# Kernel optimization log

Measured on AMD Instinct MI355X. Metric: run time of the kernel, lower is better.

Reference implementation:

```python
import jax, jax.numpy as jnp
import numpy as np
import math

H = 8      # n_heads
D = 64     # d_model (per-head dim in this module)
QDIM = 512


def setup_inputs() -> dict:
    key = jax.random.key(0)
    ks = jax.random.split(key, 11)
    B, L = 4, 1024
    s = 1.0 / math.sqrt(QDIM)
    inp = {
        "q": jax.random.normal(ks[0], (B, L, QDIM), jnp.float32),
        "k": jax.random.normal(ks[1], (B, L, QDIM), jnp.float32),
        "v": jax.random.normal(ks[2], (B, L, QDIM), jnp.float32),
        # Linear weights (torch layout: [out, in]); biases init to zeros in original
        "wq": jax.random.normal(ks[3], (H * D, QDIM), jnp.float32) * s,
        "bq": jnp.zeros((H * D,), jnp.float32),
        "wk": jax.random.normal(ks[4], (H * D, QDIM), jnp.float32) * s,
        "bk": jnp.zeros((H * D,), jnp.float32),
        "wv": jax.random.normal(ks[5], (H * D, QDIM), jnp.float32) * s,
        "bv": jnp.zeros((H * D,), jnp.float32),
        "wp": jax.random.normal(ks[6], (D, H * D), jnp.float32) * (1.0 / math.sqrt(H * D)),
        "bp": jnp.zeros((D,), jnp.float32),
    }
    return inp


def reference(q, k, v, wq, bq, wk, bk, wv, bv, wp, bp):
    b = q.shape[0]
    # projections, split into heads: [b, L, H, D] -> [b, H, L, D]
    q_s = (q @ wq.T + bq).reshape(b, -1, H, D).transpose(0, 2, 1, 3)
    k_s = (k @ wk.T + bk).reshape(b, -1, H, D).transpose(0, 2, 1, 3)
    v_s = (v @ wv.T + bv).reshape(b, -1, H, D).transpose(0, 2, 1, 3)
    # NOTE: original scales by sqrt(batch_size), not sqrt(d_k)
    scores = jnp.einsum("bhqd,bhkd->bhqk", q_s, k_s) / math.sqrt(b)
    attn = jax.nn.softmax(scores, axis=-1)
    # context = attn^T @ v  (quirk: output seq length = k_len)
    context = jnp.einsum("bhqk,bhqd->bhkd", attn, v_s)
    context = context.transpose(0, 2, 1, 3).reshape(b, -1, H * D)
    output = context @ wp.T + bp  # dropout is identity at eval
    return (output, attn)
```

## Files before the change

### kernel.cpp

```cpp
#include <hip/hip_runtime.h>

#define QD 512
#define NW (512*512)

typedef __attribute__((ext_vector_type(8))) short bf16x8;
typedef __attribute__((ext_vector_type(4))) short bf16x4;
typedef __attribute__((ext_vector_type(4))) float f32x4;

#define MFMA16(a,b,c) __builtin_amdgcn_mfma_f32_16x16x32_bf16((a),(b),(c),0,0,0)

static __device__ __forceinline__ short f2bf(float f) {
  unsigned u = __float_as_uint(f);
  u += 0x7fffu + ((u >> 16) & 1u);
  return (short)(u >> 16);
}
static __device__ __forceinline__ float bf2f(short s) {
  return __uint_as_float(((unsigned)(unsigned short)s) << 16);
}
static __device__ __forceinline__ unsigned pk2(float a, float b) {
  return (unsigned)(unsigned short)f2bf(a) | (((unsigned)(unsigned short)f2bf(b)) << 16);
}

#define GL2LDS16(g, l)                                                        \
  __builtin_amdgcn_global_load_lds(                                           \
      (const __attribute__((address_space(1))) unsigned int*)(g),             \
      (__attribute__((address_space(3))) unsigned int*)(l), 16, 0, 0)

__global__ __launch_bounds__(256) void k_wconv(
    const float* __restrict__ wq, const float* __restrict__ wk,
    const float* __restrict__ wv, const float* __restrict__ wp,
    short* __restrict__ W, short* __restrict__ WPH) {
  int i = blockIdx.x * 256 + threadIdx.x;
  if (i < NW) {
    float f = wq[i]; short h = f2bf(f);
    W[i] = h; W[NW + i] = f2bf(f - bf2f(h));
  } else if (i < 2 * NW) {
    int j = i - NW;
    float f = wk[j]; short h = f2bf(f);
    W[2 * NW + j] = h; W[3 * NW + j] = f2bf(f - bf2f(h));
  } else if (i < 3 * NW) {
    int j = i - 2 * NW;
    W[4 * NW + j] = f2bf(wv[j]);
  } else {
    int j = i - 3 * NW;
    if (j < 64 * QD) WPH[j] = f2bf(wp[j]);
  }
}

__global__ __launch_bounds__(256) void k_xconv(
    const float* __restrict__ q, const float* __restrict__ k, const float* __restrict__ v,
    short* __restrict__ XqH, short* __restrict__ XqL,
    short* __restrict__ XkH, short* __restrict__ XkL, short* __restrict__ XvH) {
  int i = blockIdx.x * 256 + threadIdx.x;
  int t = i >> 18;
  int j = i & 0x3FFFF;
  const float* src = t == 0 ? q : (t == 1 ? k : v);
  f32x4 x0 = *(const f32x4*)(src + (size_t)j * 8);
  f32x4 x1 = *(const f32x4*)(src + (size_t)j * 8 + 4);
  bf16x8 H, L;
#pragma unroll
  for (int jj = 0; jj < 4; ++jj) {
    short h0 = f2bf(x0[jj]); H[jj] = h0; L[jj] = f2bf(x0[jj] - bf2f(h0));
    short h1 = f2bf(x1[jj]); H[jj + 4] = h1; L[jj + 4] = f2bf(x1[jj] - bf2f(h1));
  }
  if (t == 0)      { *(bf16x8*)(XqH + (size_t)j * 8) = H; *(bf16x8*)(XqL + (size_t)j * 8) = L; }
  else if (t == 1) { *(bf16x8*)(XkH + (size_t)j * 8) = H; *(bf16x8*)(XkL + (size_t)j * 8) = L; }
  else             { *(bf16x8*)(XvH + (size_t)j * 8) = H; }
}

__global__ __launch_bounds__(256) void k_proj(
    const short* __restrict__ XH, const short* __restrict__ XL,
    const short* __restrict__ WH, const short* __restrict__ WL,
    const float* __restrict__ bias,
    short* __restrict__ outH, short* __restrict__ outL,
    short* __restrict__ Vt, int mode, float scale) {
  __shared__ __align__(16) short Ah[64 * 32], Al[64 * 32], Bh[64 * 32], Bl[64 * 32];
  const int tid = threadIdx.x;
  const int lane = tid & 63;
  const int col = lane & 15, g = lane >> 4;
  const int w = tid >> 6, wr = w >> 1, wc = w & 1;
  const int h = blockIdx.x;
  const int m0 = blockIdx.y * 64;
  const int srow = tid >> 2;
  const int scol = ((tid & 3) ^ (srow & 3)) * 8;
  const size_t xrow = (size_t)(m0 + srow) * QD + scol;
  const size_t wrow = (size_t)(h * 64 + srow) * QD + scol;

  f32x4 zero = {0.f, 0.f, 0.f, 0.f};
  f32x4 acc[2][2] = {{zero, zero}, {zero, zero}};

  for (int kc = 0; kc < 16; ++kc) {
    const int kb = kc * 32;
    GL2LDS16(XH + xrow + kb, &Ah[tid * 8]);
    GL2LDS16(WH + wrow + kb, &Bh[tid * 8]);
    if (mode == 0) {
      GL2LDS16(XL + xrow + kb, &Al[tid * 8]);
      GL2LDS16(WL + wrow + kb, &Bl[tid * 8]);
    }
    __syncthreads();

    bf16x8 a_h[2], a_l[2], b_h[2], b_l[2];
#pragma unroll
    for (int mt = 0; mt < 2; ++mt) {
      int rowa = wr * 32 + mt * 16 + col;
      int off = rowa * 32 + ((g ^ (rowa & 3)) * 8);
      a_h[mt] = *(const bf16x8*)&Ah[off];
      if (mode == 0) a_l[mt] = *(const bf16x8*)&Al[off];
    }
#pragma unroll
    for (int nt = 0; nt < 2; ++nt) {
      int rowb = wc * 32 + nt * 16 + col;
      int off = rowb * 32 + ((g ^ (rowb & 3)) * 8);
      b_h[nt] = *(const bf16x8*)&Bh[off];
      if (mode == 0) b_l[nt] = *(const bf16x8*)&Bl[off];
    }
#pragma unroll
    for (int mt = 0; mt < 2; ++mt)
#pragma unroll
      for (int nt = 0; nt < 2; ++nt) {
        acc[mt][nt] = MFMA16(a_h[mt], b_h[nt], acc[mt][nt]);
        if (mode == 0) {
          acc[mt][nt] = MFMA16(a_l[mt], b_h[nt], acc[mt][nt]);
          acc[mt][nt] = MFMA16(a_h[mt], b_l[nt], acc[mt][nt]);
        }
      }
    __syncthreads();
  }

#pragma unroll
  for (int nt = 0; nt < 2; ++nt) {
    int d = wc * 32 + nt * 16 + col;
    float bias_v = bias[h * 64 + d];
#pragma unroll
    for (int mt = 0; mt < 2; ++mt)
#pragma unroll
      for (int r = 0; r < 4; ++r) {
        int m = m0 + wr * 32 + mt * 16 + g * 4 + r;
        int b = m >> 10, l = m & 1023;
        float val = (acc[mt][nt][r] + bias_v) * scale;
        if (mode == 0) {
          size_t idx = (((size_t)b * 8 + h) * 1024 + l) * 64 + d;
          short hh = f2bf(val);
          outH[idx] = hh;
          outL[idx] = f2bf(val - bf2f(hh));
        } else {
          Vt[(((size_t)b * 8 + h) * 64 + d) * 1024 + l] = f2bf(val);
        }
      }
  }
}

__global__ __launch_bounds__(256) void k_sums(
    const short* __restrict__ QsH, const short* __restrict__ KsH,
    float* __restrict__ invp) {
  __shared__ __align__(16) short KL[32 * 64];
  const int tid = threadIdx.x;
  const int lane = tid & 63, w = tid >> 6;
  const int col = lane & 15, g = lane >> 4;
  int wgid = blockIdx.x + gridDim.x * blockIdx.y;
  int nid = (wgid & 7) * 64 + (wgid >> 3);
  const int qblk = nid & 15, bh = nid >> 4;
  const int q0 = qblk * 64 + w * 16;
  const size_t base = (size_t)bh * 65536;

  const short* qp = QsH + base + (size_t)(q0 + col) * 64 + g * 8;
  bf16x8 qB0 = *(const bf16x8*)qp;
  bf16x8 qB1 = *(const bf16x8*)(qp + 32);

  const int srow = tid >> 3, sslot = tid & 7;
  const short* ksrc = KsH + base + (size_t)srow * 64 + ((sslot ^ (srow & 7)) * 8);

  f32x4 zero = {0.f, 0.f, 0.f, 0.f};
  float sum = 0.f;
  for (int kb = 0; kb < 32; ++kb) {
    GL2LDS16(ksrc + kb * 2048, &KL[tid * 8]);
    __syncthreads();
#pragma unroll
    for (int sub = 0; sub < 2; ++sub) {
      const short* lb = &KL[(sub * 16 + col) * 64];
      bf16x8 ka0 = *(const bf16x8*)(lb + ((g ^ (col & 7)) * 8));
      bf16x8 ka1 = *(const bf16x8*)(lb + (((4 + g) ^ (col & 7)) * 8));
      f32x4 S = zero;
      S = MFMA16(ka0, qB0, S);
      S = MFMA16(ka1, qB1, S);
      sum += __expf(S[0]) + __expf(S[1]) + __expf(S[2]) + __expf(S[3]);
    }
    __syncthreads();
  }
  sum += __shfl_xor(sum, 16);
  sum += __shfl_xor(sum, 32);
  if (lane < 16) invp[bh * 1024 + q0 + col] = 1.f / sum;
}

__global__ __launch_bounds__(256) void k_pv(
    const short* __restrict__ QsH, const short* __restrict__ QsL,
    const short* __restrict__ KsH, const short* __restrict__ KsL,
    const short* __restrict__ Vt, const float* __restrict__ invp,
    float* __restrict__ attn, short* __restrict__ ctx) {
  __shared__ __align__(16) short QH[32 * 64], QL[32 * 64];
  const int tid = threadIdx.x;
  const int lane = tid & 63, w = tid >> 6;
  const int col = lane & 15, g = lane >> 4;
  int wgid = blockIdx.x + gridDim.x * blockIdx.y;
  int nid = (wgid & 7) * 64 + (wgid >> 3);
  const int kblk = nid & 15, bh = nid >> 4;
  const int k0 = kblk * 64 + w * 16;
  const size_t base = (size_t)bh * 65536;

  const short* kp = KsH + base + (size_t)(k0 + col) * 64 + g * 8;
  bf16x8 khB0 = *(const bf16x8*)kp;
  bf16x8 khB1 = *(const bf16x8*)(kp + 32);
  const short* kpl = KsL + base + (size_t)(k0 + col) * 64 + g * 8;
  bf16x8 klB0 = *(const bf16x8*)kpl;
  bf16x8 klB1 = *(const bf16x8*)(kpl + 32);

  const short* vb = Vt + base;
  float* ab = attn + (size_t)bh * 1024 * 1024;
  const float* invB = invp + bh * 1024;

  const int srow = tid >> 3, sslot = tid & 7;
  const size_t qsrc = base + (size_t)srow * 64 + ((sslot ^ (srow & 7)) * 8);

  f32x4 zero = {0.f, 0.f, 0.f, 0.f};
  f32x4 O[4] = {zero, zero, zero, zero};

  for (int cc = 0; cc < 32; ++cc) {
    GL2LDS16(QsH + qsrc + cc * 2048, &QH[tid * 8]);
    GL2LDS16(QsL + qsrc + cc * 2048, &QL[tid * 8]);
    __syncthreads();

    float p[2][4];
#pragma unroll
    for (int t = 0; t < 2; ++t) {
      const short* lh = &QH[(t * 16 + col) * 64];
      const short* ll = &QL[(t * 16 + col) * 64];
      int o0 = (g ^ (col & 7)) * 8, o1 = ((4 + g) ^ (col & 7)) * 8;
      bf16x8 qh0 = *(const bf16x8*)(lh + o0);
      bf16x8 qh1 = *(const bf16x8*)(lh + o1);
      bf16x8 ql0 = *(const bf16x8*)(ll + o0);
      bf16x8 ql1 = *(const bf16x8*)(ll + o1);
      f32x4 S = zero;
      S = MFMA16(qh0, khB0, S);
      S = MFMA16(qh1, khB1, S);
      S = MFMA16(ql0, khB0, S);
      S = MFMA16(ql1, khB1, S);
      S = MFMA16(qh0, klB0, S);
      S = MFMA16(qh1, klB1, S);
      f32x4 iv = *(const f32x4*)(invB + cc * 32 + t * 16 + 4 * g);
      float* ap = ab + (size_t)(cc * 32 + t * 16 + 4 * g) * 1024 + k0 + col;
#pragma unroll
      for (int r = 0; r < 4; ++r) {
        p[t][r] = __expf(S[r]) * iv[r];
        ap[(size_t)r * 1024] = p[t][r];
      }
    }
    union { bf16x8 v; unsigned u[4]; } pa;
    pa.u[0] = pk2(p[0][0], p[0][1]); pa.u[1] = pk2(p[0][2], p[0][3]);
    pa.u[2] = pk2(p[1][0], p[1][1]); pa.u[3] = pk2(p[1][2], p[1][3]);
#pragma unroll
    for (int dt = 0; dt < 4; ++dt) {
      const short* vr = vb + (size_t)(dt * 16 + col) * 1024 + cc * 32 + 4 * g;
      union { bf16x8 v; bf16x4 h[2]; } vf;
      vf.h[0] = *(const bf16x4*)vr;
      vf.h[1] = *(const bf16x4*)(vr + 16);
      O[dt] = MFMA16(pa.v, vf.v, O[dt]);
    }
    __syncthreads();
  }

  int b = bh >> 3, h = bh & 7;
#pragma unroll
  for (int dt = 0; dt < 4; ++dt)
#pragma unroll
    for (int r = 0; r < 4; ++r) {
      int kk = k0 + 4 * g + r;
      ctx[((size_t)(b * 1024 + kk)) * 512 + h * 64 + dt * 16 + col] = f2bf(O[dt][r]);
    }
}

__global__ __launch_bounds__(256) void k_out(
    const short* __restrict__ ctx, const short* __restrict__ WPH,
    const float* __restrict__ bp, float* __restrict__ out) {
  const int lane = threadIdx.x & 63, w = threadIdx.x >> 6;
  const int col = lane & 15, g = lane >> 4;
  const int m0 = blockIdx.x * 64 + w * 16;

  f32x4 zero = {0.f, 0.f, 0.f, 0.f};
  f32x4 acc[4] = {zero, zero, zero, zero};

  for (int kc = 0; kc < 16; ++kc) {
    bf16x8 a = *(const bf16x8*)(ctx + (size_t)(m0 + col) * 512 + kc * 32 + g * 8);
#pragma unroll
    for (int nt = 0; nt < 4; ++nt) {
      bf16x8 bfr = *(const bf16x8*)(WPH + (size_t)(nt * 16 + col) * 512 + kc * 32 + g * 8);
      acc[nt] = MFMA16(a, bfr, acc[nt]);
    }
  }
#pragma unroll
  for (int nt = 0; nt < 4; ++nt) {
    float bias = bp[nt * 16 + col];
#pragma unroll
    for (int r = 0; r < 4; ++r)
      out[(size_t)(m0 + g * 4 + r) * 64 + nt * 16 + col] = acc[nt][r] + bias;
  }
}

extern "C" void kernel_launch(void* const* d_in, const int* in_sizes, int n_in,
                              void* d_out, int out_size, void* d_ws, size_t ws_size,
                              hipStream_t stream) {
  const float* q  = (const float*)d_in[0];
  const float* k  = (const float*)d_in[1];
  const float* v  = (const float*)d_in[2];
  const float* wq = (const float*)d_in[3];
  const float* bq = (const float*)d_in[4];
  const float* wk = (const float*)d_in[5];
  const float* bk = (const float*)d_in[6];
  const float* wv = (const float*)d_in[7];
  const float* bv = (const float*)d_in[8];
  const float* wp = (const float*)d_in[9];
  const float* bp = (const float*)d_in[10];

  float* out  = (float*)d_out;
  float* attn = out + 262144;

  short* S = (short*)d_ws;
  const size_t E = 2097152;
  short* XqH = S;
  short* XqL = S + E;
  short* XkH = S + 2 * E;
  short* XkL = S + 3 * E;
  short* XvH = S + 4 * E;
  short* QsH = S + 5 * E;
  short* QsL = S + 6 * E;
  short* KsH = S;
  short* KsL = S + E;
  short* Vt  = S + 2 * E;
  short* ctx = S + 3 * E;
  short* W   = S + 7 * E;
  short* WPH = W + 5 * (size_t)NW;
  float* invp = (float*)(WPH + 64 * QD);

  k_wconv<<<dim3(3200), dim3(256), 0, stream>>>(wq, wk, wv, wp, W, WPH);
  k_xconv<<<dim3(3072), dim3(256), 0, stream>>>(q, k, v, XqH, XqL, XkH, XkL, XvH);
  k_proj <<<dim3(8, 64), dim3(256), 0, stream>>>(XqH, XqL, W, W + NW, bq,
                                                 QsH, QsL, nullptr, 0, 0.5f);
  k_proj <<<dim3(8, 64), dim3(256), 0, stream>>>(XkH, XkL, W + 2 * NW, W + 3 * NW, bk,
                                                 KsH, KsL, nullptr, 0, 1.0f);
  k_proj <<<dim3(8, 64), dim3(256), 0, stream>>>(XvH, XvH, W + 4 * NW, W + 4 * NW, bv,
                                                 nullptr, nullptr, Vt, 1, 1.0f);
  k_sums <<<dim3(16, 32), dim3(256), 0, stream>>>(QsH, KsH, invp);
  k_pv   <<<dim3(16, 32), dim3(256), 0, stream>>>(QsH, QsL, KsH, KsL, Vt, invp,
                                                  attn, ctx);
  k_out  <<<dim3(64), dim3(256), 0, stream>>>(ctx, WPH, bp, out);
}
```

Before: 305.8 us.

## Split softmax sums and PV over key/query chunks, reduce partial contexts

The row-sum kernel is split four ways along the key dimension, with partial sums combined through atomics and inverted in a new small kernel. The PV kernel is split along the query dimension into up to four fp32 partial context buffers, chosen by available workspace, and a new reduction kernel adds them and writes hi/lo bf16 context. The output projection now uses a three-term split-bf16 product for higher precision. This raises grid sizes from 512 blocks so more CUs are busy, at the cost of extra launches, a memset, atomics and extra fp32 traffic.

Result: slower. 319.5 us (+4.5%).

```diff
diff --git a/kernel.cpp b/kernel.cpp
--- a/kernel.cpp
+++ b/kernel.cpp
@@ -29,7 +29,7 @@
 __global__ __launch_bounds__(256) void k_wconv(
     const float* __restrict__ wq, const float* __restrict__ wk,
     const float* __restrict__ wv, const float* __restrict__ wp,
-    short* __restrict__ W, short* __restrict__ WPH) {
+    short* __restrict__ W, short* __restrict__ WPH, short* __restrict__ WPL) {
   int i = blockIdx.x * 256 + threadIdx.x;
   if (i < NW) {
     float f = wq[i]; short h = f2bf(f);
@@ -43,7 +43,10 @@
     W[4 * NW + j] = f2bf(wv[j]);
   } else {
     int j = i - 3 * NW;
-    if (j < 64 * QD) WPH[j] = f2bf(wp[j]);
+    if (j < 64 * QD) {
+      float f = wp[j]; short h = f2bf(f);
+      WPH[j] = h; WPL[j] = f2bf(f - bf2f(h));
+    }
   }
 }
 
@@ -152,7 +155,7 @@
 
 __global__ __launch_bounds__(256) void k_sums(
     const short* __restrict__ QsH, const short* __restrict__ KsH,
-    float* __restrict__ invp) {
+    float* __restrict__ sums) {
   __shared__ __align__(16) short KL[32 * 64];
   const int tid = threadIdx.x;
   const int lane = tid & 63, w = tid >> 6;
@@ -160,6 +163,7 @@
   int wgid = blockIdx.x + gridDim.x * blockIdx.y;
   int nid = (wgid & 7) * 64 + (wgid >> 3);
   const int qblk = nid & 15, bh = nid >> 4;
+  const int kq = blockIdx.z;
   const int q0 = qblk * 64 + w * 16;
   const size_t base = (size_t)bh * 65536;
 
@@ -168,11 +172,12 @@
   bf16x8 qB1 = *(const bf16x8*)(qp + 32);
 
   const int srow = tid >> 3, sslot = tid & 7;
-  const short* ksrc = KsH + base + (size_t)srow * 64 + ((sslot ^ (srow & 7)) * 8);
+  const short* ksrc = KsH + base + (size_t)(kq * 256 + srow) * 64 +
+                      ((sslot ^ (srow & 7)) * 8);
 
   f32x4 zero = {0.f, 0.f, 0.f, 0.f};
   float sum = 0.f;
-  for (int kb = 0; kb < 32; ++kb) {
+  for (int kb = 0; kb < 8; ++kb) {
     GL2LDS16(ksrc + kb * 2048, &KL[tid * 8]);
     __syncthreads();
 #pragma unroll
@@ -189,14 +194,21 @@
   }
   sum += __shfl_xor(sum, 16);
   sum += __shfl_xor(sum, 32);
-  if (lane < 16) invp[bh * 1024 + q0 + col] = 1.f / sum;
+  if (lane < 16) atomicAdd(&sums[bh * 1024 + q0 + col], sum);
+}
+
+__global__ __launch_bounds__(256) void k_inv(float* __restrict__ s) {
+  int i = blockIdx.x * 256 + threadIdx.x;
+  s[i] = 1.f / s[i];
 }
 
 __global__ __launch_bounds__(256) void k_pv(
     const short* __restrict__ QsH, const short* __restrict__ QsL,
     const short* __restrict__ KsH, const short* __restrict__ KsL,
     const short* __restrict__ Vt, const float* __restrict__ invp,
-    float* __restrict__ attn, short* __restrict__ ctx) {
+    float* __restrict__ attn,
+    float* __restrict__ c0, float* __restrict__ c1,
+    float* __restrict__ c2, float* __restrict__ c3, int cpb) {
   __shared__ __align__(16) short QH[32 * 64], QL[32 * 64];
   const int tid = threadIdx.x;
   const int lane = tid & 63, w = tid >> 6;
@@ -204,6 +216,8 @@
   int wgid = blockIdx.x + gridDim.x * blockIdx.y;
   int nid = (wgid & 7) * 64 + (wgid >> 3);
   const int kblk = nid & 15, bh = nid >> 4;
+  const int qc = blockIdx.z;
+  float* ctxP = qc == 0 ? c0 : (qc == 1 ? c1 : (qc == 2 ? c2 : c3));
   const int k0 = kblk * 64 + w * 16;
   const size_t base = (size_t)bh * 65536;
 
@@ -224,7 +238,8 @@
   f32x4 zero = {0.f, 0.f, 0.f, 0.f};
   f32x4 O[4] = {zero, zero, zero, zero};
 
-  for (int cc = 0; cc < 32; ++cc) {
+  for (int ci = 0; ci < cpb; ++ci) {
+    const int cc = qc * cpb + ci;
     GL2LDS16(QsH + qsrc + cc * 2048, &QH[tid * 8]);
     GL2LDS16(QsL + qsrc + cc * 2048, &QL[tid * 8]);
     __syncthreads();
@@ -274,12 +289,33 @@
 #pragma unroll
     for (int r = 0; r < 4; ++r) {
       int kk = k0 + 4 * g + r;
-      ctx[((size_t)(b * 1024 + kk)) * 512 + h * 64 + dt * 16 + col] = f2bf(O[dt][r]);
-    }
+      ctxP[((size_t)(b * 1024 + kk)) * 512 + h * 64 + dt * 16 + col] = O[dt][r];
+    }
+}
+
+__global__ __launch_bounds__(256) void k_red(
+    const float* __restrict__ c0, const float* __restrict__ c1,
+    const float* __restrict__ c2, const float* __restrict__ c3, int nc,
+    short* __restrict__ ctxH, short* __restrict__ ctxL) {
+  size_t i = ((size_t)blockIdx.x * 256 + threadIdx.x) * 8;
+  f32x4 a0 = *(const f32x4*)(c0 + i);
+  f32x4 a1 = *(const f32x4*)(c0 + i + 4);
+  if (nc > 1) { a0 += *(const f32x4*)(c1 + i); a1 += *(const f32x4*)(c1 + i + 4); }
+  if (nc > 2) { a0 += *(const f32x4*)(c2 + i); a1 += *(const f32x4*)(c2 + i + 4);
+                a0 += *(const f32x4*)(c3 + i); a1 += *(const f32x4*)(c3 + i + 4); }
+  bf16x8 H, L;
+#pragma unroll
+  for (int j = 0; j < 4; ++j) {
+    short h0 = f2bf(a0[j]); H[j] = h0; L[j] = f2bf(a0[j] - bf2f(h0));
+    short h1 = f2bf(a1[j]); H[j + 4] = h1; L[j + 4] = f2bf(a1[j] - bf2f(h1));
+  }
+  *(bf16x8*)(ctxH + i) = H;
+  *(bf16x8*)(ctxL + i) = L;
 }
 
 __global__ __launch_bounds__(256) void k_out(
-    const short* __restrict__ ctx, const short* __restrict__ WPH,
+    const short* __restrict__ ctxH, const short* __restrict__ ctxL,
+    const short* __restrict__ WPH, const short* __restrict__ WPL,
     const float* __restrict__ bp, float* __restrict__ out) {
   const int lane = threadIdx.x & 63, w = threadIdx.x >> 6;
   const int col = lane & 15, g = lane >> 4;
@@ -289,11 +325,17 @@
   f32x4 acc[4] = {zero, zero, zero, zero};
 
   for (int kc = 0; kc < 16; ++kc) {
-    bf16x8 a = *(const bf16x8*)(ctx + (size_t)(m0 + col) * 512 + kc * 32 + g * 8);
+    size_t aoff = (size_t)(m0 + col) * 512 + kc * 32 + g * 8;
+    bf16x8 a_h = *(const bf16x8*)(ctxH + aoff);
+    bf16x8 a_l = *(const bf16x8*)(ctxL + aoff);
 #pragma unroll
     for (int nt = 0; nt < 4; ++nt) {
-      bf16x8 bfr = *(const bf16x8*)(WPH + (size_t)(nt * 16 + col) * 512 + kc * 32 + g * 8);
-      acc[nt] = MFMA16(a, bfr, acc[nt]);
+      size_t boff = (size_t)(nt * 16 + col) * 512 + kc * 32 + g * 8;
+      bf16x8 b_h = *(const bf16x8*)(WPH + boff);
+      bf16x8 b_l = *(const bf16x8*)(WPL + boff);
+      acc[nt] = MFMA16(a_h, b_h, acc[nt]);
+      acc[nt] = MFMA16(a_l, b_h, acc[nt]);
+      acc[nt] = MFMA16(a_h, b_l, acc[nt]);
     }
   }
 #pragma unroll
@@ -335,12 +377,25 @@
   short* KsH = S;
   short* KsL = S + E;
   short* Vt  = S + 2 * E;
-  short* ctx = S + 3 * E;
+  short* ctxH = S;
+  short* ctxL = S + E;
   short* W   = S + 7 * E;
   short* WPH = W + 5 * (size_t)NW;
-  float* invp = (float*)(WPH + 64 * QD);
-
-  k_wconv<<<dim3(3200), dim3(256), 0, stream>>>(wq, wk, wv, wp, W, WPH);
+  short* WPL = WPH + 64 * QD;
+  float* sums = (float*)(WPL + 64 * QD);
+  float* ctxP0 = (float*)(S + 3 * E);
+  char*  tail = (char*)(sums + 32768);
+  size_t used = (size_t)(tail - (char*)d_ws);
+  size_t avail = ws_size > used ? ws_size - used : 0;
+  const size_t CB = (size_t)8 * 1024 * 1024;
+  int NC = avail >= 3 * CB ? 4 : (avail >= CB ? 2 : 1);
+  float* c1 = NC > 1 ? (float*)tail : ctxP0;
+  float* c2 = NC > 3 ? (float*)(tail + CB) : ctxP0;
+  float* c3 = NC > 3 ? (float*)(tail + 2 * CB) : ctxP0;
+  int cpb = 32 / NC;
+
+  hipMemsetAsync(sums, 0, 32768 * sizeof(float), stream);
+  k_wconv<<<dim3(3200), dim3(256), 0, stream>>>(wq, wk, wv, wp, W, WPH, WPL);
   k_xconv<<<dim3(3072), dim3(256), 0, stream>>>(q, k, v, XqH, XqL, XkH, XkL, XvH);
   k_proj <<<dim3(8, 64), dim3(256), 0, stream>>>(XqH, XqL, W, W + NW, bq,
                                                  QsH, QsL, nullptr, 0, 0.5f);
@@ -348,8 +403,10 @@
                                                  KsH, KsL, nullptr, 0, 1.0f);
   k_proj <<<dim3(8, 64), dim3(256), 0, stream>>>(XvH, XvH, W + 4 * NW, W + 4 * NW, bv,
                                                  nullptr, nullptr, Vt, 1, 1.0f);
-  k_sums <<<dim3(16, 32), dim3(256), 0, stream>>>(QsH, KsH, invp);
-  k_pv   <<<dim3(16, 32), dim3(256), 0, stream>>>(QsH, QsL, KsH, KsL, Vt, invp,
-                                                  attn, ctx);
-  k_out  <<<dim3(64), dim3(256), 0, stream>>>(ctx, WPH, bp, out);
-}
+  k_sums <<<dim3(16, 32, 4), dim3(256), 0, stream>>>(QsH, KsH, sums);
+  k_inv  <<<dim3(128), dim3(256), 0, stream>>>(sums);
+  k_pv   <<<dim3(16, 32, NC), dim3(256), 0, stream>>>(QsH, QsL, KsH, KsL, Vt, sums,
+                                                      attn, ctxP0, c1, c2, c3, cpb);
+  k_red  <<<dim3(1024), dim3(256), 0, stream>>>(ctxP0, c1, c2, c3, NC, ctxH, ctxL);
+  k_out  <<<dim3(64), dim3(256), 0, stream>>>(ctxH, ctxL, WPH, WPL, bp, out);
+}
```
